# Optimization experiments

Measured on AMD Instinct MI355X. Metric: run time of the kernel, lower is better.

The kernel has to match this reference:

```python
import jax, jax.numpy as jnp
import numpy as np

N = 1024   # num_nodes
D = 128    # embedding_size


def setup_inputs() -> dict:
    key = jax.random.key(0)
    k1, k2, k3 = jax.random.split(key, 3)
    z = jax.random.normal(k1, (N, D), dtype=jnp.float32)
    # torch.nn.Linear(2D, D): weight [D, 2D]; stored here as W1 [2D, D] for x @ W1
    W1 = jax.random.normal(k2, (2 * D, D), dtype=jnp.float32) * (1.0 / np.sqrt(2 * D))
    b1 = jnp.zeros((D,), dtype=jnp.float32)
    W2 = jax.random.normal(k3, (D, 1), dtype=jnp.float32) * (1.0 / np.sqrt(D))
    b2 = jnp.zeros((1,), dtype=jnp.float32)
    return {"z": z, "W1": W1, "b1": b1, "W2": W2, "b2": b2}


def reference(z, W1, b1, W2, b2):
    # Original: z_i = z.repeat_interleave(N) (i varies slowly),
    #           z_j = z.repeat(N)            (j varies fast),
    # q = Linear2(relu(Linear1(cat[z_i, z_j]))).squeeze()  -> shape [N*N]
    # Equivalent split-linear form (cat @ W1 == z_i @ W1[:D] + z_j @ W1[D:]):
    d = z.shape[1]
    pi = z @ W1[:d]          # [N, D] projection of left node
    pj = z @ W1[d:]          # [N, D] projection of right node
    h = jax.nn.relu(pi[:, None, :] + pj[None, :, :] + b1)  # [N, N, D]
    q = (h @ W2).squeeze(-1) + b2                          # [N, N]
    return q.reshape(-1)     # pair k = i*N + j, matching repeat_interleave/repeat order
```

## Files before the change

### kernel.cpp

```cpp
#include <hip/hip_runtime.h>
#include <hip/hip_bf16.h>


#define NN 1024
#define DD 128
#define TI 64
#define TJ 64
#define PAD 132

__global__ __launch_bounds__(256) void proj_kernel(
    const float* __restrict__ z,
    const float* __restrict__ W1,
    const float* __restrict__ b1,
    float* __restrict__ pic,
    float* __restrict__ pj)
{
    __shared__ float zs[DD];
    const int i = blockIdx.x;
    const int t = threadIdx.x;
    if (t < DD) zs[t] = z[i * DD + t];
    __syncthreads();

    const int half = t >> 7;
    const int d = t & (DD - 1);
    const float* Wcol = W1 + half * DD * DD + d;

    float acc = 0.f;
    #pragma unroll 16
    for (int k = 0; k < DD; ++k)
        acc = fmaf(zs[k], Wcol[k * DD], acc);

    if (half == 0)
        pic[i * DD + d] = acc + b1[d];
    else
        pj[i * DD + d] = acc;
}

__global__ __launch_bounds__(256) void pair_kernel(
    const float* __restrict__ pic,
    const float* __restrict__ pj,
    const float* __restrict__ W2,
    const float* __restrict__ b2,
    float* __restrict__ out)
{
    __shared__ float a_s[TI * PAD];
    __shared__ float b_s[TJ * PAD];
    __shared__ float w_s[DD];

    const int t  = threadIdx.x;
    const int bi = blockIdx.x;
    const int bj = blockIdx.y;

    const float4* srcA = (const float4*)(pic + bi * TI * DD);
    const float4* srcB = (const float4*)(pj + bj * TJ * DD);
    #pragma unroll
    for (int u = 0; u < 8; ++u) {
        int f   = t + 256 * u;
        int row = f >> 5;
        int c4  = f & 31;
        float4 va = srcA[f];
        float4 vb = srcB[f];
        *(float4*)&a_s[row * PAD + c4 * 4] = va;
        *(float4*)&b_s[row * PAD + c4 * 4] = vb;
    }
    if (t < DD) w_s[t] = W2[t];
    __syncthreads();

    const int tx = t & 15;
    const int ty = t >> 4;
    const float* ap = a_s + ty * PAD;
    const float* bp = b_s + tx * PAD;

    float acc[4][4];
    #pragma unroll
    for (int ii = 0; ii < 4; ++ii)
        #pragma unroll
        for (int jj = 0; jj < 4; ++jj) acc[ii][jj] = 0.f;

    #pragma unroll 2
    for (int d = 0; d < DD; d += 4) {
        float4 w4 = *(const float4*)(w_s + d);
        float4 av[4], bv[4];
        #pragma unroll
        for (int ii = 0; ii < 4; ++ii) av[ii] = *(const float4*)(ap + ii * 16 * PAD + d);
        #pragma unroll
        for (int jj = 0; jj < 4; ++jj) bv[jj] = *(const float4*)(bp + jj * 16 * PAD + d);

        #pragma unroll
        for (int ii = 0; ii < 4; ++ii) {
            const float ax = av[ii].x, ay = av[ii].y, az = av[ii].z, aw = av[ii].w;
            #pragma unroll
            for (int jj = 0; jj < 4; ++jj) {
                acc[ii][jj] = fmaf(fmaxf(ax + bv[jj].x, 0.f), w4.x, acc[ii][jj]);
                acc[ii][jj] = fmaf(fmaxf(ay + bv[jj].y, 0.f), w4.y, acc[ii][jj]);
                acc[ii][jj] = fmaf(fmaxf(az + bv[jj].z, 0.f), w4.z, acc[ii][jj]);
                acc[ii][jj] = fmaf(fmaxf(aw + bv[jj].w, 0.f), w4.w, acc[ii][jj]);
            }
        }
    }

    const float bb = b2[0];
    #pragma unroll
    for (int ii = 0; ii < 4; ++ii) {
        const int i = bi * TI + ty + ii * 16;
        #pragma unroll
        for (int jj = 0; jj < 4; ++jj) {
            const int j = bj * TJ + tx + jj * 16;
            out[(size_t)i * NN + j] = acc[ii][jj] + bb;
        }
    }
}

extern "C" void kernel_launch(void* const* d_in, const int* in_sizes, int n_in,
                              void* d_out, int out_size, void* d_ws, size_t ws_size,
                              hipStream_t stream)
{
    const float* z  = (const float*)d_in[0];
    const float* W1 = (const float*)d_in[1];
    const float* b1 = (const float*)d_in[2];
    const float* W2 = (const float*)d_in[3];
    const float* b2 = (const float*)d_in[4];
    float* out = (float*)d_out;

    float* pic = (float*)d_ws;
    float* pj  = pic + NN * DD;

    proj_kernel<<<NN, 256, 0, stream>>>(z, W1, b1, pic, pj);

    dim3 grid(NN / TI, NN / TJ);
    pair_kernel<<<grid, 256, 0, stream>>>(pic, pj, W2, b2, out);
}
```

Baseline: 82.03 us.

## Halve pair tile width, register-block projection over four rows, read W2 directly

The pair kernel's J tile shrinks from 64 to 32, so each thread computes a 4x2 output block and the grid doubles to 512 blocks for better CU coverage on the MI355X. It also sets a launch-bounds occupancy hint, fully unrolls the D loop, and reads W2 straight from global memory instead of staging it in LDS. The projection kernel now computes four rows per block and reuses each W1 load across them, which quarters its grid and its W1 traffic. The price is lower per-thread arithmetic intensity in the pair kernel (more LDS loads per FMA) and uncached-looking W2 loads inside the hot loop.

After: 79.54 us. 1.03x faster.

```diff
diff --git a/kernel.cpp b/kernel.cpp
--- a/kernel.cpp
+++ b/kernel.cpp
@@ -1,11 +1,10 @@
 #include <hip/hip_runtime.h>
-#include <hip/hip_bf16.h>
 
 
 #define NN 1024
 #define DD 128
 #define TI 64
-#define TJ 64
+#define TJ 32
 #define PAD 132
 
 __global__ __launch_bounds__(256) void proj_kernel(
@@ -15,28 +14,37 @@
     float* __restrict__ pic,
     float* __restrict__ pj)
 {
-    __shared__ float zs[DD];
-    const int i = blockIdx.x;
+    const int i0 = blockIdx.x * 4;
     const int t = threadIdx.x;
-    if (t < DD) zs[t] = z[i * DD + t];
-    __syncthreads();
-
     const int half = t >> 7;
     const int d = t & (DD - 1);
-    const float* Wcol = W1 + half * DD * DD + d;
+    const float* __restrict__ Wcol = W1 + half * DD * DD + d;
+    const float* __restrict__ z0 = z + i0 * DD;
 
-    float acc = 0.f;
-    #pragma unroll 16
-    for (int k = 0; k < DD; ++k)
-        acc = fmaf(zs[k], Wcol[k * DD], acc);
-
-    if (half == 0)
-        pic[i * DD + d] = acc + b1[d];
-    else
-        pj[i * DD + d] = acc;
+    float a0 = 0.f, a1 = 0.f, a2 = 0.f, a3 = 0.f;
+    #pragma unroll 8
+    for (int k = 0; k < DD; ++k) {
+        const float w = Wcol[k * DD];
+        a0 = fmaf(z0[k], w, a0);
+        a1 = fmaf(z0[DD + k], w, a1);
+        a2 = fmaf(z0[2 * DD + k], w, a2);
+        a3 = fmaf(z0[3 * DD + k], w, a3);
+    }
+    if (half == 0) {
+        const float bb = b1[d];
+        pic[(i0 + 0) * DD + d] = a0 + bb;
+        pic[(i0 + 1) * DD + d] = a1 + bb;
+        pic[(i0 + 2) * DD + d] = a2 + bb;
+        pic[(i0 + 3) * DD + d] = a3 + bb;
+    } else {
+        pj[(i0 + 0) * DD + d] = a0;
+        pj[(i0 + 1) * DD + d] = a1;
+        pj[(i0 + 2) * DD + d] = a2;
+        pj[(i0 + 3) * DD + d] = a3;
+    }
 }
 
-__global__ __launch_bounds__(256) void pair_kernel(
+__global__ __launch_bounds__(256, 2) void pair_kernel(
     const float* __restrict__ pic,
     const float* __restrict__ pj,
     const float* __restrict__ W2,
@@ -45,25 +53,27 @@
 {
     __shared__ float a_s[TI * PAD];
     __shared__ float b_s[TJ * PAD];
-    __shared__ float w_s[DD];
 
     const int t  = threadIdx.x;
     const int bi = blockIdx.x;
     const int bj = blockIdx.y;
 
-    const float4* srcA = (const float4*)(pic + bi * TI * DD);
-    const float4* srcB = (const float4*)(pj + bj * TJ * DD);
+    const float4* __restrict__ srcA = (const float4*)(pic + bi * TI * DD);
+    const float4* __restrict__ srcB = (const float4*)(pj + bj * TJ * DD);
     #pragma unroll
     for (int u = 0; u < 8; ++u) {
         int f   = t + 256 * u;
         int row = f >> 5;
         int c4  = f & 31;
-        float4 va = srcA[f];
-        float4 vb = srcB[f];
-        *(float4*)&a_s[row * PAD + c4 * 4] = va;
-        *(float4*)&b_s[row * PAD + c4 * 4] = vb;
+        *(float4*)&a_s[row * PAD + c4 * 4] = srcA[f];
     }
-    if (t < DD) w_s[t] = W2[t];
+    #pragma unroll
+    for (int u = 0; u < 4; ++u) {
+        int f   = t + 256 * u;
+        int row = f >> 5;
+        int c4  = f & 31;
+        *(float4*)&b_s[row * PAD + c4 * 4] = srcB[f];
+    }
     __syncthreads();
 
     const int tx = t & 15;
@@ -71,26 +81,26 @@
     const float* ap = a_s + ty * PAD;
     const float* bp = b_s + tx * PAD;
 
-    float acc[4][4];
+    float acc[4][2];
     #pragma unroll
     for (int ii = 0; ii < 4; ++ii)
         #pragma unroll
-        for (int jj = 0; jj < 4; ++jj) acc[ii][jj] = 0.f;
+        for (int jj = 0; jj < 2; ++jj) acc[ii][jj] = 0.f;
 
-    #pragma unroll 2
+    #pragma unroll
     for (int d = 0; d < DD; d += 4) {
-        float4 w4 = *(const float4*)(w_s + d);
-        float4 av[4], bv[4];
+        const float4 w4 = *(const float4*)(W2 + d);
+        float4 av[4], bv[2];
         #pragma unroll
         for (int ii = 0; ii < 4; ++ii) av[ii] = *(const float4*)(ap + ii * 16 * PAD + d);
         #pragma unroll
-        for (int jj = 0; jj < 4; ++jj) bv[jj] = *(const float4*)(bp + jj * 16 * PAD + d);
+        for (int jj = 0; jj < 2; ++jj) bv[jj] = *(const float4*)(bp + jj * 16 * PAD + d);
 
         #pragma unroll
         for (int ii = 0; ii < 4; ++ii) {
             const float ax = av[ii].x, ay = av[ii].y, az = av[ii].z, aw = av[ii].w;
             #pragma unroll
-            for (int jj = 0; jj < 4; ++jj) {
+            for (int jj = 0; jj < 2; ++jj) {
                 acc[ii][jj] = fmaf(fmaxf(ax + bv[jj].x, 0.f), w4.x, acc[ii][jj]);
                 acc[ii][jj] = fmaf(fmaxf(ay + bv[jj].y, 0.f), w4.y, acc[ii][jj]);
                 acc[ii][jj] = fmaf(fmaxf(az + bv[jj].z, 0.f), w4.z, acc[ii][jj]);
@@ -104,7 +114,7 @@
     for (int ii = 0; ii < 4; ++ii) {
         const int i = bi * TI + ty + ii * 16;
         #pragma unroll
-        for (int jj = 0; jj < 4; ++jj) {
+        for (int jj = 0; jj < 2; ++jj) {
             const int j = bj * TJ + tx + jj * 16;
             out[(size_t)i * NN + j] = acc[ii][jj] + bb;
         }
@@ -125,7 +135,7 @@
     float* pic = (float*)d_ws;
     float* pj  = pic + NN * DD;
 
-    proj_kernel<<<NN, 256, 0, stream>>>(z, W1, b1, pic, pj);
+    proj_kernel<<<NN / 4, 256, 0, stream>>>(z, W1, b1, pic, pj);
 
     dim3 grid(NN / TI, NN / TJ);
     pair_kernel<<<grid, 256, 0, stream>>>(pic, pj, W2, b2, out);
```
